# Optimization experiments

Hardware: AMD Instinct MI355X
Metric: run time of the kernel (lower is better)

## Reference

```python
import jax, jax.numpy as jnp
import numpy as np

B, G, C = 32, 50, 80
IMG = 640
STRIDES = (8, 16, 32)
CENTER_RADIUS = 2.5


def _make_grids():
    xs, ys, ss = [], [], []
    for s in STRIDES:
        n = IMG // s
        yv, xv = np.meshgrid(np.arange(n, dtype=np.float32), np.arange(n, dtype=np.float32), indexing='ij')
        xs.append(xv.reshape(-1)); ys.append(yv.reshape(-1))
        ss.append(np.full(n * n, s, dtype=np.float32))
    return np.concatenate(xs), np.concatenate(ys), np.concatenate(ss)


def setup_inputs():
    xg, yg, sg = _make_grids()
    A = xg.shape[0]  # 8400
    ks = jax.random.split(jax.random.key(0), 5)
    # decoded box predictions near grid centers (cxcywh, pixel units)
    ctr = jnp.stack([jnp.asarray((xg + 0.5) * sg), jnp.asarray((yg + 0.5) * sg)], -1)[None] \
        + jax.random.normal(ks[0], (B, A, 2)) * 8.0
    wh = jnp.exp(jax.random.normal(ks[1], (B, A, 2)) * 0.5) * jnp.asarray(sg)[None, :, None] * 4.0
    pred_output = jnp.concatenate([ctr, wh, jax.random.normal(ks[2], (B, A, 1 + C))], -1)  # [B,A,85]
    obj_preds = jax.random.normal(ks[3], (B, A, 1))
    cls_preds = jax.random.normal(ks[4], (B, A, C))
    # labels [B,G,5] = (class, cx, cy, w, h); first num_gt rows valid, rest zero
    rng = np.random.RandomState(0)
    lab = np.zeros((B, G, 5), np.float32)
    for b in range(B):
        ng = rng.randint(5, G)
        lab[b, :ng, 0] = rng.randint(0, C, ng)
        lab[b, :ng, 1:3] = rng.uniform(40.0, IMG - 40.0, (ng, 2))
        lab[b, :ng, 3:5] = rng.uniform(20.0, 160.0, (ng, 2))
    return {"pred_output": pred_output, "obj_preds": obj_preds, "cls_preds": cls_preds,
            "labels": jnp.asarray(lab), "x_shifts": jnp.asarray(xg),
            "y_shifts": jnp.asarray(yg), "strides": jnp.asarray(sg)}


def _pairwise_iou_cxcywh(a, b):
    # a [G,4], b [A,4] -> [G,A]
    tl = jnp.maximum(a[:, None, :2] - a[:, None, 2:] * 0.5, b[None, :, :2] - b[None, :, 2:] * 0.5)
    br = jnp.minimum(a[:, None, :2] + a[:, None, 2:] * 0.5, b[None, :, :2] + b[None, :, 2:] * 0.5)
    area_a = a[:, 2] * a[:, 3]
    area_b = b[:, 2] * b[:, 3]
    en = jnp.all(tl < br, -1).astype(a.dtype)
    area_i = jnp.prod(br - tl, -1) * en
    return area_i / (area_a[:, None] + area_b[None, :] - area_i + 1e-16)


def _assign_one(gt, gt_valid, boxes, cls_logit, obj_logit, xg, yg, sg):
    # SimOTA assignment for a single image, fully vectorized over [G,A].
    # gt [G,5], gt_valid [G], boxes [A,4], cls_logit [A,C], obj_logit [A,1]
    num_gt = gt.shape[0]
    gt_cls = gt[:, 0].astype(jnp.int32)
    gb = gt[:, 1:5]
    xc = (xg + 0.5) * sg
    yc = (yg + 0.5) * sg
    d_box = jnp.stack([
        xc[None, :] - (gb[:, 0:1] - gb[:, 2:3] * 0.5),
        (gb[:, 0:1] + gb[:, 2:3] * 0.5) - xc[None, :],
        yc[None, :] - (gb[:, 1:2] - gb[:, 3:4] * 0.5),
        (gb[:, 1:2] + gb[:, 3:4] * 0.5) - yc[None, :]], -1)
    in_boxes = (jnp.min(d_box, -1) > 0) & gt_valid[:, None]
    d_ctr = jnp.stack([
        xc[None, :] - (gb[:, 0:1] - CENTER_RADIUS * sg[None, :]),
        (gb[:, 0:1] + CENTER_RADIUS * sg[None, :]) - xc[None, :],
        yc[None, :] - (gb[:, 1:2] - CENTER_RADIUS * sg[None, :]),
        (gb[:, 1:2] + CENTER_RADIUS * sg[None, :]) - yc[None, :]], -1)
    in_ctr = (jnp.min(d_ctr, -1) > 0) & gt_valid[:, None]
    fg0 = jnp.any(in_boxes | in_ctr, 0)           # [A] candidate anchors (fg_mask)
    and_ctr = in_boxes & in_ctr                    # [G,A]
    ious = _pairwise_iou_cxcywh(gb, boxes) * fg0[None, :].astype(boxes.dtype) * gt_valid[:, None].astype(boxes.dtype)
    # pairwise BCE(sqrt(sig(cls)*sig(obj)), one_hot) summed over classes, without [G,A,C]
    logq = 0.5 * (jax.nn.log_sigmoid(cls_logit) + jax.nn.log_sigmoid(obj_logit))  # [A,C]
    q = jnp.clip(jnp.exp(logq), 1e-7, 1.0 - 1e-7)
    s_neg = jnp.sum(jnp.log1p(-q), -1)             # [A] sum_c log(1-q_c)
    q_gt = q[:, gt_cls].T                          # [G,A]
    cls_cost = -jnp.log(q_gt) + jnp.log1p(-q_gt) - s_neg[None, :]
    invalid = (~fg0)[None, :] | (~gt_valid)[:, None]
    cost = cls_cost - 3.0 * jnp.log(ious + 1e-8) + 1e5 * (~and_ctr) + 1e9 * invalid
    # dynamic-k: sum of top-10 ious per gt, truncated, min 1
    dyn_k = jnp.maximum(jnp.sum(jax.lax.top_k(ious, 10)[0], -1).astype(jnp.int32), 1)  # [G]
    ranks = jnp.argsort(jnp.argsort(cost, 1), 1)   # rank of each anchor in ascending cost
    matching = (ranks < dyn_k[:, None]) & gt_valid[:, None]
    # resolve anchors claimed by >1 gt: keep min-cost gt
    best_gt = jnp.argmin(cost, 0)                  # [A]
    onehot_best = jnp.arange(num_gt)[:, None] == best_gt[None, :]
    matching = jnp.where(jnp.sum(matching, 0)[None, :] > 1, onehot_best, matching)
    fg = jnp.any(matching, 0)                      # [A] final fg mask
    matched = jnp.argmax(matching, 0)              # [A] matched gt index
    pred_iou = jnp.sum(matching * ious, 0)         # [A]
    cls_t = jax.nn.one_hot(gt_cls[matched], cls_logit.shape[-1], dtype=boxes.dtype) \
        * (pred_iou * fg.astype(boxes.dtype))[:, None]
    return cls_t, fg, matched


def _forward(pred_output, obj_preds, cls_preds, labels, x_shifts, y_shifts, strides):
    bbox = pred_output[:, :, :4]
    gt_valid = labels.sum(-1) > 0
    cls_t, fg, matched = jax.vmap(_assign_one, in_axes=(0, 0, 0, 0, 0, None, None, None))(
        labels, gt_valid, bbox, cls_preds, obj_preds, x_shifts, y_shifts, strides)
    cls_t = jax.lax.stop_gradient(cls_t)  # get_assignments is @torch.no_grad()
    reg_t = jnp.take_along_axis(labels[:, :, 1:5], matched[:, :, None], axis=1)  # [B,A,4]
    fg_f = fg.astype(pred_output.dtype)
    num_fg = jnp.maximum(jnp.sum(fg_f), 1.0)
    # IoU loss (cxcywh), loss = 1 - iou^2, only on fg anchors
    tl = jnp.maximum(bbox[..., :2] - bbox[..., 2:] * 0.5, reg_t[..., :2] - reg_t[..., 2:] * 0.5)
    br = jnp.minimum(bbox[..., :2] + bbox[..., 2:] * 0.5, reg_t[..., :2] + reg_t[..., 2:] * 0.5)
    en = jnp.all(tl < br, -1).astype(bbox.dtype)
    area_i = jnp.prod(br - tl, -1) * en
    area_u = bbox[..., 2] * bbox[..., 3] + reg_t[..., 2] * reg_t[..., 3] - area_i
    iou = area_i / (area_u + 1e-16)
    loss_iou = jnp.sum((1.0 - iou ** 2) * fg_f) / num_fg
    bce = lambda x, y: jax.nn.softplus(x) - x * y  # BCEWithLogits, reduction='none'
    loss_obj = jnp.sum(bce(obj_preds[..., 0], fg_f)) / num_fg
    loss_cls = jnp.sum(bce(cls_preds, cls_t) * fg_f[..., None]) / num_fg
    return 5.0 * loss_iou + loss_obj + loss_cls


def reference(pred_output, obj_preds, cls_preds, labels, x_shifts, y_shifts, strides):
    return _forward(pred_output, obj_preds, cls_preds, labels, x_shifts, y_shifts, strides)
```

## Files before the change

### kernel.cpp

```cpp
#include <hip/hip_runtime.h>
#include <cstdint>
#include <cstddef>

#define BB 32
#define GG 50
#define CC 80
#define AA 8400
#define PCH (5 + CC)
#define NLB ((BB * AA + 255) / 256)
#define FGBIT 63
#define SENTC 3.3e38f
#define SENTI 0x7fffffff

__device__ __forceinline__ float logsig_fast(float x) {
    float e = __expf(-fabsf(x));
    return fminf(x, 0.f) - __logf(1.f + e);
}
__device__ __forceinline__ float softplusf(float x) {
    return fmaxf(x, 0.f) + log1pf(expf(-fabsf(x)));
}

__device__ __forceinline__ float pair_iou(float px, float py, float pw, float ph,
                                          float gx, float gy, float gw, float gh) {
    float tlx = fmaxf(gx - gw * 0.5f, px - pw * 0.5f);
    float tly = fmaxf(gy - gh * 0.5f, py - ph * 0.5f);
    float brx = fminf(gx + gw * 0.5f, px + pw * 0.5f);
    float bry = fminf(gy + gh * 0.5f, py + ph * 0.5f);
    float en = (tlx < brx && tly < bry) ? 1.f : 0.f;
    float ai = (brx - tlx) * (bry - tly) * en;
    return ai / (gw * gh + pw * ph - ai + 1e-16f);
}
__device__ __forceinline__ float cost_val(float x , float lo ,
                                          float sn , float v ,
                                          bool ac, bool f0, bool valid) {
    float lq = 0.5f * (logsig_fast(x) + lo);
    float q = fminf(fmaxf(__expf(lq), 1e-7f), 1.f - 1e-7f);
    float cst = -__logf(q) + __logf(1.f - q) - sn;
    cst -= 3.0f * __logf(v + 1e-8f);
    cst += 100000.0f * (ac ? 0.f : 1.f);
    cst += 1000000000.0f * ((!f0 || !valid) ? 1.f : 0.f);
    return cst;
}

__global__ __launch_bounds__(256)
void k_precompute(const float* __restrict__ pred, const float* __restrict__ obj,
                  const float* __restrict__ cls,
                  float2* __restrict__ lsn, float* __restrict__ sps,
                  float4* __restrict__ pbox) {
    int t = blockIdx.x * blockDim.x + threadIdx.x;
    int i = t >> 2;
    int sub = t & 3;
    if (i >= BB * AA) return;
    float lo = logsig_fast(obj[i]);
    float K = __expf(0.5f * lo);
    const float4* c4 = (const float4*)(cls + (size_t)i * CC);
    float smax = 0.f, psp = 1.f, p1 = 1.f, p2 = 1.f;
#pragma unroll
    for (int j = 0; j < 5; j++) {
        float4 v = c4[sub + 4 * j];
        float xs4[4] = {v.x, v.y, v.z, v.w};
        float pg = 1.f;
#pragma unroll
        for (int u = 0; u < 4; u++) {
            float x = xs4[u];
            float th = __expf(-0.5f * fabsf(x));
            float t2 = th * th;
            smax += fmaxf(x, 0.f);
            psp *= (1.f + t2);
            float qq = K * (x < 0.f ? th : 1.f) * rsqrtf(1.f + t2);
            qq = fminf(fmaxf(qq, 1e-7f), 1.f - 1e-7f);
            pg *= (1.f - qq);
        }
        if (j < 2) p1 *= pg; else p2 *= pg;
    }
    float sp = smax + __logf(psp);
    float sn = __logf(p1) + __logf(p2);
    sp += __shfl_xor(sp, 1); sn += __shfl_xor(sn, 1);
    sp += __shfl_xor(sp, 2); sn += __shfl_xor(sn, 2);
    float pv = pred[(size_t)i * PCH + sub];
    ((float*)pbox)[(size_t)i * 4 + sub] = pv;
    if (sub == 0) {
        lsn[i] = make_float2(lo, sn);
        sps[i] = sp;
    }
}

__global__ void k_geom(const float* __restrict__ labels, const float* __restrict__ xs,
                       const float* __restrict__ ys, const float* __restrict__ ss,
                       const float4* __restrict__ pbox, const float2* __restrict__ lsn,
                       unsigned long long* __restrict__ amask,
                       int* __restrict__ clist, unsigned long long* __restrict__ camask,
                       float4* __restrict__ cpbox, float2* __restrict__ clsn,
                       int* __restrict__ ccnt) {
    int b = blockIdx.y;
    int a = blockIdx.x * blockDim.x + threadIdx.x;
    __shared__ float lab[GG * 5];
    __shared__ int lv[GG];
    for (int t = threadIdx.x; t < GG * 5; t += blockDim.x) lab[t] = labels[b * GG * 5 + t];
    __syncthreads();
    if (threadIdx.x < GG) {
        const float* r = lab + threadIdx.x * 5;
        lv[threadIdx.x] = ((r[0] + r[1] + r[2] + r[3] + r[4]) > 0.f) ? 1 : 0;
    }
    __syncthreads();
    if (a >= AA) return;
    float s = ss[a];
    float xc = (xs[a] + 0.5f) * s;
    float yc = (ys[a] + 0.5f) * s;
    unsigned long long m = 0;
    int any = 0;
    for (int g = 0; g < GG; g++) {
        if (!lv[g]) continue;
        const float* r = lab + g * 5;
        float gx = r[1], gy = r[2], gw = r[3], gh = r[4];
        float d1 = xc - (gx - gw * 0.5f);
        float d2 = (gx + gw * 0.5f) - xc;
        float d3 = yc - (gy - gh * 0.5f);
        float d4 = (gy + gh * 0.5f) - yc;
        bool ib = fminf(fminf(d1, d2), fminf(d3, d4)) > 0.f;
        float cr = 2.5f * s;
        float e1 = xc - (gx - cr);
        float e2 = (gx + cr) - xc;
        float e3 = yc - (gy - cr);
        float e4 = (gy + cr) - yc;
        bool ic = fminf(fminf(e1, e2), fminf(e3, e4)) > 0.f;
        if (ib || ic) any = 1;
        if (ib && ic) m |= 1ull << g;
    }
    if (any) m |= 1ull << FGBIT;
    amask[b * AA + a] = m;
    int lane = threadIdx.x & 63;
    unsigned long long act = __ballot(m != 0);
    if (act) {
        int leader = __ffsll(act) - 1;
        int base = 0;
        if (lane == leader) base = atomicAdd(&ccnt[b], __popcll(act));
        base = __shfl(base, leader);
        if (m != 0) {
            int off = __popcll(act & ((1ull << lane) - 1ull));
            int pos = b * AA + base + off;
            clist[pos] = a;
            camask[pos] = m;
            cpbox[pos] = pbox[b * AA + a];
            clsn[pos] = lsn[b * AA + a];
        }
    }
}

__global__ __launch_bounds__(256, 4)
void k_assign(const float4* __restrict__ pbox, const float2* __restrict__ lsn,
              const float* __restrict__ cls,
              const unsigned long long* __restrict__ amask,
              const float* __restrict__ labels,
              const int* __restrict__ clist, const unsigned long long* __restrict__ camask,
              const float4* __restrict__ cpbox, const float2* __restrict__ clsn,
              const int* __restrict__ ccnt,
              unsigned long long* __restrict__ mmask) {
    int w = blockIdx.x;
    int b = w / GG, g = w % GG;
    const float* r = labels + (size_t)w * 5;
    float gcls = r[0], gx = r[1], gy = r[2], gw = r[3], gh = r[4];
    if (!((gcls + gx + gy + gw + gh) > 0.f)) return;
    int gtc = (int)gcls;
    int tid = threadIdx.x;
    int lane = tid & 63;
    int wv = tid >> 6;
    int cnt = ccnt[b];

    float ivl[10];
    float cvl[10];
    int   cil[10];
#pragma unroll
    for (int t = 0; t < 10; t++) { ivl[t] = 0.f; cvl[t] = SENTC; cil[t] = SENTI; }
    int nlc = 0;

    for (int i0 = wv * 64 + lane; i0 < cnt; i0 += 256) {
        int pos = b * AA + i0;
        unsigned long long am = camask[pos];
        float4 pb = cpbox[pos];
        bool ac = (am >> g) & 1ull;
        nlc += ac ? 1 : 0;
        float v = pair_iou(pb.x, pb.y, pb.z, pb.w, gx, gy, gw, gh);
        if (v > ivl[9]) {
            float mv = v;
#pragma unroll
            for (int t = 0; t < 10; t++)
                if (mv > ivl[t]) { float tmp = ivl[t]; ivl[t] = mv; mv = tmp; }
        }
        if (ac) {
            int a = clist[pos];
            float2 ls = clsn[pos];
            float c = cost_val(cls[((size_t)b * AA + a) * CC + gtc], ls.x, ls.y, v,
                               true, true, true);
            int id = a;
            if (c < cvl[9] || (c == cvl[9] && id < cil[9])) {
#pragma unroll
                for (int t = 0; t < 10; t++) {
                    bool sw = (c < cvl[t]) || (c == cvl[t] && id < cil[t]);
                    if (sw) {
                        float tf = cvl[t]; cvl[t] = c; c = tf;
                        int ti = cil[t]; cil[t] = id; id = ti;
                    }
                }
            }
        }
    }

    __shared__ float IV[4][10];
    __shared__ float CV[4][10];
    __shared__ int CI[4][10];
    __shared__ int NAC[4];
    __shared__ int s_k, s_n0;
    __shared__ int sel[10];

    {
        int s = nlc;
#pragma unroll
        for (int off = 1; off < 64; off <<= 1) s += __shfl_xor(s, off);
        if (lane == 0) NAC[wv] = s;
    }

    for (int rr = 0; rr < 10; rr++) {
        float bv = ivl[0];
        int bl = lane;
#pragma unroll
        for (int off = 1; off < 64; off <<= 1) {
            float ov = __shfl_xor(bv, off);
            int ol = __shfl_xor(bl, off);
            if (ov > bv || (ov == bv && ol < bl)) { bv = ov; bl = ol; }
        }
        if (lane == 0) IV[wv][rr] = bv;
        if (lane == bl) {
#pragma unroll
            for (int t = 0; t < 9; t++) ivl[t] = ivl[t + 1];
            ivl[9] = 0.f;
        }
    }

    for (int rr = 0; rr < 10; rr++) {
        float bc = cvl[0];
        int bi = cil[0];
        int bl = lane;
#pragma unroll
        for (int off = 1; off < 64; off <<= 1) {
            float oc = __shfl_xor(bc, off);
            int oi = __shfl_xor(bi, off);
            int ol = __shfl_xor(bl, off);
            bool tk = (oc < bc) || (oc == bc && (oi < bi || (oi == bi && ol < bl)));
            if (tk) { bc = oc; bi = oi; bl = ol; }
        }
        if (lane == 0) { CV[wv][rr] = bc; CI[wv][rr] = bi; }
        if (lane == bl) {
#pragma unroll
            for (int t = 0; t < 9; t++) { cvl[t] = cvl[t + 1]; cil[t] = cil[t + 1]; }
            cvl[9] = SENTC; cil[9] = SENTI;
        }
    }
    __syncthreads();

    if (tid == 0) {
        int h[4] = {0, 0, 0, 0};
        float ssum = 0.f;
        for (int j = 0; j < 10; j++) {
            float bv = -1.f; int bc = 0;
#pragma unroll
            for (int c2 = 0; c2 < 4; c2++)
                if (h[c2] < 10 && IV[c2][h[c2]] > bv) { bv = IV[c2][h[c2]]; bc = c2; }
            ssum += bv;
            h[bc]++;
        }
        int k = (int)ssum;
        if (k < 1) k = 1;
        s_k = k;
        s_n0 = NAC[0] + NAC[1] + NAC[2] + NAC[3];
    }
    __syncthreads();
    int k = s_k;

    if (s_n0 < k) {
#pragma unroll
        for (int t = 0; t < 10; t++) { cvl[t] = SENTC; cil[t] = SENTI; }
        const int chunk = AA / 4;
        int abase = wv * chunk, aend = abase + chunk;
        for (int a0 = abase; a0 < aend; a0 += 64) {
            int a = a0 + lane;
            bool inr = a < aend;
            int ia = b * AA + (inr ? a : (aend - 1));
            unsigned long long am = amask[ia];
            bool f0 = inr && ((am >> FGBIT) & 1ull);
            bool ac = inr && ((am >> g) & 1ull);
            float v = 0.f;
            if (f0) {
                float4 pb = pbox[ia];
                v = pair_iou(pb.x, pb.y, pb.z, pb.w, gx, gy, gw, gh);
            }
            float c = SENTC; int id = SENTI;
            if (inr) {
                float x = cls[(size_t)ia * CC + gtc];
                float2 ls = lsn[ia];
                c = cost_val(x, ls.x, ls.y, v, ac, f0, true);
                id = a;
            }
            if (c < cvl[9] || (c == cvl[9] && id < cil[9])) {
#pragma unroll
                for (int t = 0; t < 10; t++) {
                    bool sw = (c < cvl[t]) || (c == cvl[t] && id < cil[t]);
                    if (sw) {
                        float tf = cvl[t]; cvl[t] = c; c = tf;
                        int ti = cil[t]; cil[t] = id; id = ti;
                    }
                }
            }
        }
        for (int rr = 0; rr < 10; rr++) {
            float bc = cvl[0];
            int bi = cil[0];
            int bl = lane;
#pragma unroll
            for (int off = 1; off < 64; off <<= 1) {
                float oc = __shfl_xor(bc, off);
                int oi = __shfl_xor(bi, off);
                int ol = __shfl_xor(bl, off);
                bool tk = (oc < bc) || (oc == bc && (oi < bi || (oi == bi && ol < bl)));
                if (tk) { bc = oc; bi = oi; bl = ol; }
            }
            if (lane == 0) { CV[wv][rr] = bc; CI[wv][rr] = bi; }
            if (lane == bl) {
#pragma unroll
                for (int t = 0; t < 9; t++) { cvl[t] = cvl[t + 1]; cil[t] = cil[t + 1]; }
                cvl[9] = SENTC; cil[9] = SENTI;
            }
        }
        __syncthreads();
    }

    if (tid == 0) {
        int h[4] = {0, 0, 0, 0};
        for (int j = 0; j < k; j++) {
            float bv = SENTC; int bix = SENTI; int bc = 0;
#pragma unroll
            for (int c2 = 0; c2 < 4; c2++) {
                if (h[c2] < 10) {
                    float av = CV[c2][h[c2]]; int ax = CI[c2][h[c2]];
                    if (av < bv || (av == bv && ax < bix)) { bv = av; bix = ax; bc = c2; }
                }
            }
            sel[j] = bix;
            h[bc]++;
        }
    }
    __syncthreads();
    if (tid < k) {
        atomicOr(&mmask[(size_t)b * AA + sel[tid]], 1ull << g);
    }
}

__global__ void k_loss(const float4* __restrict__ pbox, const float* __restrict__ obj,
                       const float* __restrict__ cls, const float* __restrict__ labels,
                       const float2* __restrict__ lsn,
                       const unsigned long long* __restrict__ amask,
                       const unsigned long long* __restrict__ mmask,
                       const float* __restrict__ sps, float* __restrict__ partial) {
    int i = blockIdx.x * blockDim.x + threadIdx.x;
    int i_first = blockIdx.x * blockDim.x;
    int i_last = min(i_first + (int)blockDim.x - 1, BB * AA - 1);
    int b0 = i_first / AA, b1 = i_last / AA;
    __shared__ float lab[2][GG * 5];
    for (int t = threadIdx.x; t < GG * 5; t += blockDim.x) {
        lab[0][t] = labels[(size_t)b0 * GG * 5 + t];
        lab[1][t] = labels[(size_t)b1 * GG * 5 + t];
    }
    __syncthreads();

    float li = 0.f, lo = 0.f, lc = 0.f, nf = 0.f;
    if (i < BB * AA) {
        int b = i / AA, a = i % AA;
        const float* lb = lab[(b == b0) ? 0 : 1];
        unsigned long long m = mmask[i];
        int cnt = __popcll(m);
        bool fg = (m != 0);
        int mg = 0;
        float4 pb = pbox[i];
        unsigned long long am = amask[i];
        bool f0 = (am >> FGBIT) & 1ull;
        if (cnt > 1) {
            float2 ls = lsn[i];
            float bv = 3.4e38f;
            for (int g = 0; g < GG; g++) {
                const float* r = lb + g * 5;
                float gcls = r[0], gx = r[1], gy = r[2], gw = r[3], gh = r[4];
                bool valid = (gcls + gx + gy + gw + gh) > 0.f;
                int gtc = (int)gcls;
                float raw = pair_iou(pb.x, pb.y, pb.z, pb.w, gx, gy, gw, gh);
                float v = raw * (f0 ? 1.f : 0.f) * (valid ? 1.f : 0.f);
                float x = cls[(size_t)i * CC + gtc];
                bool ac = (am >> g) & 1ull;
                float cst = cost_val(x, ls.x, ls.y, v, ac, f0, valid);
                if (cst < bv) { bv = cst; mg = g; }
            }
        } else if (cnt == 1) {
            mg = __ffsll((unsigned long long)m) - 1;
        }
        float o = obj[i];
        lo = softplusf(o) - (fg ? o : 0.f);
        if (fg) {
            const float* r = lb + mg * 5;
            float gcls = r[0], gx = r[1], gy = r[2], gw = r[3], gh = r[4];
            bool valid = (gcls + gx + gy + gw + gh) > 0.f;
            int gtc = (int)gcls;
            float piou = pair_iou(pb.x, pb.y, pb.z, pb.w, gx, gy, gw, gh)
                         * (f0 ? 1.f : 0.f) * (valid ? 1.f : 0.f);
            float tlx = fmaxf(pb.x - pb.z * 0.5f, gx - gw * 0.5f);
            float tly = fmaxf(pb.y - pb.w * 0.5f, gy - gh * 0.5f);
            float brx = fminf(pb.x + pb.z * 0.5f, gx + gw * 0.5f);
            float bry = fminf(pb.y + pb.w * 0.5f, gy + gh * 0.5f);
            float en = (tlx < brx && tly < bry) ? 1.f : 0.f;
            float ai = (brx - tlx) * (bry - tly) * en;
            float u = pb.z * pb.w + gw * gh - ai;
            float v2 = ai / (u + 1e-16f);
            li = 1.f - v2 * v2;
            lc = sps[i] - cls[(size_t)i * CC + gtc] * piou;
            nf = 1.f;
        }
    }
    for (int off = 32; off; off >>= 1) {
        li += __shfl_down(li, off);
        lo += __shfl_down(lo, off);
        lc += __shfl_down(lc, off);
        nf += __shfl_down(nf, off);
    }
    __shared__ float red[4][4];
    int wid = threadIdx.x >> 6;
    if ((threadIdx.x & 63) == 0) {
        red[wid][0] = li; red[wid][1] = lo; red[wid][2] = lc; red[wid][3] = nf;
    }
    __syncthreads();
    if (threadIdx.x == 0) {
        float s0 = 0.f, s1 = 0.f, s2 = 0.f, s3 = 0.f;
#pragma unroll
        for (int t = 0; t < 4; t++) {
            s0 += red[t][0]; s1 += red[t][1]; s2 += red[t][2]; s3 += red[t][3];
        }
        ((float4*)partial)[blockIdx.x] = make_float4(s0, s1, s2, s3);
    }
}

__global__ void k_final(const float* __restrict__ partial, float* __restrict__ out) {
    int tid = threadIdx.x;
    float s0 = 0.f, s1 = 0.f, s2 = 0.f, s3 = 0.f;
    const float4* pb = (const float4*)partial;
    for (int i = tid; i < NLB; i += 256) {
        float4 v = pb[i];
        s0 += v.x; s1 += v.y; s2 += v.z; s3 += v.w;
    }
    for (int off = 32; off; off >>= 1) {
        s0 += __shfl_down(s0, off);
        s1 += __shfl_down(s1, off);
        s2 += __shfl_down(s2, off);
        s3 += __shfl_down(s3, off);
    }
    __shared__ float red[4][4];
    int wid = tid >> 6;
    if ((tid & 63) == 0) {
        red[wid][0] = s0; red[wid][1] = s1; red[wid][2] = s2; red[wid][3] = s3;
    }
    __syncthreads();
    if (tid == 0) {
        float li = 0.f, lo = 0.f, lc = 0.f, nf = 0.f;
#pragma unroll
        for (int t = 0; t < 4; t++) {
            li += red[t][0]; lo += red[t][1]; lc += red[t][2]; nf += red[t][3];
        }
        nf = fmaxf(nf, 1.f);
        out[0] = (5.f * li + lo + lc) / nf;
    }
}

extern "C" void kernel_launch(void* const* d_in, const int* in_sizes, int n_in,
                              void* d_out, int out_size, void* d_ws, size_t ws_size,
                              hipStream_t stream) {
    const float* pred = (const float*)d_in[0];
    const float* obj  = (const float*)d_in[1];
    const float* cls  = (const float*)d_in[2];
    const float* lab  = (const float*)d_in[3];
    const float* xs   = (const float*)d_in[4];
    const float* ys   = (const float*)d_in[5];
    const float* ss   = (const float*)d_in[6];
    float* out = (float*)d_out;

    const size_t BA = (size_t)BB * AA;

    float4* pbox  = (float4*)d_ws;
    float4* cpbox = pbox + BA;
    float2* lsn   = (float2*)(cpbox + BA);
    float2* clsn  = lsn + BA;
    unsigned long long* amask  = (unsigned long long*)(clsn + BA);
    unsigned long long* camask = amask + BA;
    unsigned long long* mmask  = camask + BA;
    float* sps = (float*)(mmask + BA);
    float* partial = sps + BA;
    int* clist = (int*)(partial + (size_t)NLB * 4);
    int* ccnt  = clist + BA;

    hipMemsetAsync(mmask, 0, BA * sizeof(unsigned long long), stream);
    hipMemsetAsync(ccnt, 0, BB * sizeof(int), stream);

    dim3 blk(256);
    k_precompute<<<dim3((BB * AA * 4 + 255) / 256), blk, 0, stream>>>(pred, obj, cls,
                                                                      lsn, sps, pbox);
    k_geom<<<dim3((AA + 255) / 256, BB), blk, 0, stream>>>(lab, xs, ys, ss, pbox, lsn,
                                                           amask, clist, camask, cpbox,
                                                           clsn, ccnt);
    k_assign<<<dim3(BB * GG), blk, 0, stream>>>(pbox, lsn, cls, amask, lab,
                                                clist, camask, cpbox, clsn, ccnt, mmask);
    k_loss<<<dim3(NLB), blk, 0, stream>>>(pbox, obj, cls, lab, lsn, amask,
                                          mmask, sps, partial);
    k_final<<<1, blk, 0, stream>>>(partial, out);
}
```

Measured before the change: 150.6 us.

## Run class-score precompute only on compacted candidate anchors after geometry pass

The full-size precompute kernel is removed, and a new k_pre_fg kernel runs after k_geom. It computes the obj/cls log-sum terms only for anchors in the compacted candidate list. Box coordinates are read straight from pred instead of being copied into a pbox buffer. This avoids streaming the whole class-logit tensor and the box copy for anchors that can never be foreground. The risk is that lsn/sps stay uninitialized for non-candidate anchors, which any fallback path reading them must tolerate.

```diff
diff --git a/kernel.cpp b/kernel.cpp
--- a/kernel.cpp
+++ b/kernel.cpp
@@ -42,56 +42,12 @@
     return cst;
 }
 
-__global__ __launch_bounds__(256)
-void k_precompute(const float* __restrict__ pred, const float* __restrict__ obj,
-                  const float* __restrict__ cls,
-                  float2* __restrict__ lsn, float* __restrict__ sps,
-                  float4* __restrict__ pbox) {
-    int t = blockIdx.x * blockDim.x + threadIdx.x;
-    int i = t >> 2;
-    int sub = t & 3;
-    if (i >= BB * AA) return;
-    float lo = logsig_fast(obj[i]);
-    float K = __expf(0.5f * lo);
-    const float4* c4 = (const float4*)(cls + (size_t)i * CC);
-    float smax = 0.f, psp = 1.f, p1 = 1.f, p2 = 1.f;
-#pragma unroll
-    for (int j = 0; j < 5; j++) {
-        float4 v = c4[sub + 4 * j];
-        float xs4[4] = {v.x, v.y, v.z, v.w};
-        float pg = 1.f;
-#pragma unroll
-        for (int u = 0; u < 4; u++) {
-            float x = xs4[u];
-            float th = __expf(-0.5f * fabsf(x));
-            float t2 = th * th;
-            smax += fmaxf(x, 0.f);
-            psp *= (1.f + t2);
-            float qq = K * (x < 0.f ? th : 1.f) * rsqrtf(1.f + t2);
-            qq = fminf(fmaxf(qq, 1e-7f), 1.f - 1e-7f);
-            pg *= (1.f - qq);
-        }
-        if (j < 2) p1 *= pg; else p2 *= pg;
-    }
-    float sp = smax + __logf(psp);
-    float sn = __logf(p1) + __logf(p2);
-    sp += __shfl_xor(sp, 1); sn += __shfl_xor(sn, 1);
-    sp += __shfl_xor(sp, 2); sn += __shfl_xor(sn, 2);
-    float pv = pred[(size_t)i * PCH + sub];
-    ((float*)pbox)[(size_t)i * 4 + sub] = pv;
-    if (sub == 0) {
-        lsn[i] = make_float2(lo, sn);
-        sps[i] = sp;
-    }
-}
-
 __global__ void k_geom(const float* __restrict__ labels, const float* __restrict__ xs,
                        const float* __restrict__ ys, const float* __restrict__ ss,
-                       const float4* __restrict__ pbox, const float2* __restrict__ lsn,
+                       const float* __restrict__ pred,
                        unsigned long long* __restrict__ amask,
                        int* __restrict__ clist, unsigned long long* __restrict__ camask,
-                       float4* __restrict__ cpbox, float2* __restrict__ clsn,
-                       int* __restrict__ ccnt) {
+                       float4* __restrict__ cpbox, int* __restrict__ ccnt) {
     int b = blockIdx.y;
     int a = blockIdx.x * blockDim.x + threadIdx.x;
     __shared__ float lab[GG * 5];
@@ -141,14 +97,61 @@
             int pos = b * AA + base + off;
             clist[pos] = a;
             camask[pos] = m;
-            cpbox[pos] = pbox[b * AA + a];
-            clsn[pos] = lsn[b * AA + a];
-        }
+            const float* p = pred + (size_t)(b * AA + a) * PCH;
+            cpbox[pos] = make_float4(p[0], p[1], p[2], p[3]);
+        }
+    }
+}
+
+__global__ __launch_bounds__(256)
+void k_pre_fg(const float* __restrict__ obj, const float* __restrict__ cls,
+              const int* __restrict__ clist, const int* __restrict__ ccnt,
+              float2* __restrict__ clsn, float2* __restrict__ lsn,
+              float* __restrict__ sps) {
+    int b = blockIdx.y;
+    int cnt = ccnt[b];
+    int t = blockIdx.x * blockDim.x + threadIdx.x;
+    int p = t >> 2;
+    int sub = t & 3;
+    if (p >= cnt) return;
+    int pos = b * AA + p;
+    int a = clist[pos];
+    int ia = b * AA + a;
+    float lo = logsig_fast(obj[ia]);
+    float K = __expf(0.5f * lo);
+    const float4* c4 = (const float4*)(cls + (size_t)ia * CC);
+    float smax = 0.f, psp = 1.f, p1 = 1.f, p2 = 1.f;
+#pragma unroll
+    for (int j = 0; j < 5; j++) {
+        float4 v = c4[sub + 4 * j];
+        float xs4[4] = {v.x, v.y, v.z, v.w};
+        float pg = 1.f;
+#pragma unroll
+        for (int u = 0; u < 4; u++) {
+            float x = xs4[u];
+            float th = __expf(-0.5f * fabsf(x));
+            float t2 = th * th;
+            smax += fmaxf(x, 0.f);
+            psp *= (1.f + t2);
+            float qq = K * (x < 0.f ? th : 1.f) * rsqrtf(1.f + t2);
+            qq = fminf(fmaxf(qq, 1e-7f), 1.f - 1e-7f);
+            pg *= (1.f - qq);
+        }
+        if (j < 2) p1 *= pg; else p2 *= pg;
+    }
+    float sp = smax + __logf(psp);
+    float sn = __logf(p1) + __logf(p2);
+    sp += __shfl_xor(sp, 1); sn += __shfl_xor(sn, 1);
+    sp += __shfl_xor(sp, 2); sn += __shfl_xor(sn, 2);
+    if (sub == 0) {
+        clsn[pos] = make_float2(lo, sn);
+        lsn[ia] = make_float2(lo, sn);
+        sps[ia] = sp;
     }
 }
 
 __global__ __launch_bounds__(256, 4)
-void k_assign(const float4* __restrict__ pbox, const float2* __restrict__ lsn,
+void k_assign(const float* __restrict__ pred, const float2* __restrict__ lsn,
               const float* __restrict__ cls,
               const unsigned long long* __restrict__ amask,
               const float* __restrict__ labels,
@@ -291,8 +294,8 @@
             bool ac = inr && ((am >> g) & 1ull);
             float v = 0.f;
             if (f0) {
-                float4 pb = pbox[ia];
-                v = pair_iou(pb.x, pb.y, pb.z, pb.w, gx, gy, gw, gh);
+                const float* p = pred + (size_t)ia * PCH;
+                v = pair_iou(p[0], p[1], p[2], p[3], gx, gy, gw, gh);
             }
             float c = SENTC; int id = SENTI;
             if (inr) {
@@ -355,7 +358,7 @@
     }
 }
 
-__global__ void k_loss(const float4* __restrict__ pbox, const float* __restrict__ obj,
+__global__ void k_loss(const float* __restrict__ pred, const float* __restrict__ obj,
                        const float* __restrict__ cls, const float* __restrict__ labels,
                        const float2* __restrict__ lsn,
                        const unsigned long long* __restrict__ amask,
@@ -380,7 +383,11 @@
         int cnt = __popcll(m);
         bool fg = (m != 0);
         int mg = 0;
-        float4 pb = pbox[i];
+        float4 pb = make_float4(0.f, 0.f, 0.f, 0.f);
+        if (fg) {
+            const float* p = pred + (size_t)i * PCH;
+            pb = make_float4(p[0], p[1], p[2], p[3]);
+        }
         unsigned long long am = amask[i];
         bool f0 = (am >> FGBIT) & 1ull;
         if (cnt > 1) {
@@ -490,8 +497,7 @@
 
     const size_t BA = (size_t)BB * AA;
 
-    float4* pbox  = (float4*)d_ws;
-    float4* cpbox = pbox + BA;
+    float4* cpbox = (float4*)d_ws;
     float2* lsn   = (float2*)(cpbox + BA);
     float2* clsn  = lsn + BA;
     unsigned long long* amask  = (unsigned long long*)(clsn + BA);
@@ -506,14 +512,14 @@
     hipMemsetAsync(ccnt, 0, BB * sizeof(int), stream);
 
     dim3 blk(256);
-    k_precompute<<<dim3((BB * AA * 4 + 255) / 256), blk, 0, stream>>>(pred, obj, cls,
-                                                                      lsn, sps, pbox);
-    k_geom<<<dim3((AA + 255) / 256, BB), blk, 0, stream>>>(lab, xs, ys, ss, pbox, lsn,
+    k_geom<<<dim3((AA + 255) / 256, BB), blk, 0, stream>>>(lab, xs, ys, ss, pred,
                                                            amask, clist, camask, cpbox,
-                                                           clsn, ccnt);
-    k_assign<<<dim3(BB * GG), blk, 0, stream>>>(pbox, lsn, cls, amask, lab,
+                                                           ccnt);
+    k_pre_fg<<<dim3((AA * 4 + 255) / 256, BB), blk, 0, stream>>>(obj, cls, clist, ccnt,
+                                                                 clsn, lsn, sps);
+    k_assign<<<dim3(BB * GG), blk, 0, stream>>>(pred, lsn, cls, amask, lab,
                                                 clist, camask, cpbox, clsn, ccnt, mmask);
-    k_loss<<<dim3(NLB), blk, 0, stream>>>(pbox, obj, cls, lab, lsn, amask,
+    k_loss<<<dim3(NLB), blk, 0, stream>>>(pred, obj, cls, lab, lsn, amask,
                                           mmask, sps, partial);
     k_final<<<1, blk, 0, stream>>>(partial, out);
 }
```

Result: faster. 143.2 us (-4.9%).
